# Kernel tuning notes

Measured on AMD Instinct MI355X. Metric: run time of the kernel, lower is better.

## Reference

```python
import jax, jax.numpy as jnp
import numpy as np

N_A = 50000; N_B = 50000          # nodes per type
FD = 8; BINS = 32; EMB = 16       # discrete features, bins, per-feature embed dim
HID = 64; ZD = 32                 # hidden_dim, embed_dim
E = 800000                        # edges per relation (avg degree 16)


def setup_inputs() -> dict:
    key = jax.random.key(0)
    ks = iter(jax.random.split(key, 64))
    def nrm(shape, s=0.05):
        return jax.random.normal(next(ks), shape, jnp.float32) * s
    def ri(shape, hi):
        return jax.random.randint(next(ks), shape, 0, hi, dtype=jnp.int32)
    inp = {
        'x_A': ri((N_A, FD), BINS),
        'x_B': ri((N_B, FD), BINS),
        'ei_ab': ri((2, E), N_A),   # src in A, dst in B (N_A == N_B)
        'ei_ba': ri((2, E), N_B),
        'ei_aa': ri((2, E), N_A),
        # per-feature embedding tables [FD, BINS, EMB]
        'emb_A': nrm((FD, BINS, EMB)), 'emb_B': nrm((FD, BINS, EMB)),
        # pre_lin per node type (in = FD*EMB)
        'pre_W_A': nrm((FD * EMB, HID)), 'pre_b_A': nrm((HID,)),
        'pre_W_B': nrm((FD * EMB, HID)), 'pre_b_B': nrm((HID,)),
        # SAGEConv per relation: lin_l (on aggregated msgs, with bias), lin_r (root, no bias)
        'sage_l_W_ab': nrm((HID, HID)), 'sage_l_b_ab': nrm((HID,)), 'sage_r_W_ab': nrm((HID, HID)),
        'sage_l_W_ba': nrm((HID, HID)), 'sage_l_b_ba': nrm((HID,)), 'sage_r_W_ba': nrm((HID, HID)),
        'sage_l_W_aa': nrm((HID, HID)), 'sage_l_b_aa': nrm((HID,)), 'sage_r_W_aa': nrm((HID, HID)),
        # lin_proj per node type
        'proj_W_A': nrm((HID, ZD)), 'proj_b_A': nrm((ZD,)),
        'proj_W_B': nrm((HID, ZD)), 'proj_b_B': nrm((ZD,)),
        # feature heads per node type -> FD*BINS logits
        'head_W_A': nrm((ZD, FD * BINS)), 'head_b_A': nrm((FD * BINS,)),
        'head_W_B': nrm((ZD, FD * BINS)), 'head_b_B': nrm((FD * BINS,)),
        # bilinear edge decoders per relation: W [1, ZD, ZD], bias [1]
        'bil_W_ab': nrm((1, ZD, ZD)), 'bil_b_ab': nrm((1,)),
        'bil_W_ba': nrm((1, ZD, ZD)), 'bil_b_ba': nrm((1,)),
        'bil_W_aa': nrm((1, ZD, ZD)), 'bil_b_aa': nrm((1,)),
    }
    return inp


def _segment_mean(vals, idx, n):
    s = jax.ops.segment_sum(vals, idx, num_segments=n)
    c = jax.ops.segment_sum(jnp.ones((vals.shape[0], 1), vals.dtype), idx, num_segments=n)
    return s / jnp.maximum(c, 1.0)


def _sage(x_src, x_dst, ei, Wl, bl, Wr):
    # SAGEConv: lin_l(mean_{j in N(i)} x_j) + lin_r(x_i)
    m = _segment_mean(x_src[ei[0]], ei[1], x_dst.shape[0])
    return m @ Wl + bl + x_dst @ Wr


def _embed(x, emb):
    # emb: [FD, BINS, EMB]; x: [N, FD] ints -> [N, FD*EMB]
    e = emb[jnp.arange(FD)[None, :], x]            # [N, FD, EMB]
    return e.reshape(x.shape[0], FD * EMB)


def _bilinear(zs, zd, W, b):
    # nn.Bilinear: out_o = zs^T W_o zd + b_o ; here out dim 1, squeeze
    return (jnp.einsum('ei,oij,ej->eo', zs, W, zd) + b)[:, 0]


def _forward(x_A, x_B, ei_ab, ei_ba, ei_aa,
             emb_A, emb_B, pre_W_A, pre_b_A, pre_W_B, pre_b_B,
             sage_l_W_ab, sage_l_b_ab, sage_r_W_ab,
             sage_l_W_ba, sage_l_b_ba, sage_r_W_ba,
             sage_l_W_aa, sage_l_b_aa, sage_r_W_aa,
             proj_W_A, proj_b_A, proj_W_B, proj_b_B,
             head_W_A, head_b_A, head_W_B, head_b_B,
             bil_W_ab, bil_b_ab, bil_W_ba, bil_b_ba, bil_W_aa, bil_b_aa):
    # feature encoder + pre_lin + relu
    x0_A = jax.nn.relu(_embed(x_A, emb_A) @ pre_W_A + pre_b_A)
    x0_B = jax.nn.relu(_embed(x_B, emb_B) @ pre_W_B + pre_b_B)
    # HeteroConv(SAGEConv per relation, aggr='mean' over relations per dst type)
    h_B = _sage(x0_A, x0_B, ei_ab, sage_l_W_ab, sage_l_b_ab, sage_r_W_ab)
    h_A = (_sage(x0_B, x0_A, ei_ba, sage_l_W_ba, sage_l_b_ba, sage_r_W_ba)
           + _sage(x0_A, x0_A, ei_aa, sage_l_W_aa, sage_l_b_aa, sage_r_W_aa)) * 0.5
    # projection
    z_A = jax.nn.relu(h_A @ proj_W_A + proj_b_A)
    z_B = jax.nn.relu(h_B @ proj_W_B + proj_b_B)
    # feature decode
    fl_A = (z_A @ head_W_A + head_b_A).reshape(-1, FD, BINS)
    fl_B = (z_B @ head_W_B + head_b_B).reshape(-1, FD, BINS)
    # edge decode (bilinear on gathered endpoint embeddings)
    s_ab = _bilinear(z_A[ei_ab[0]], z_B[ei_ab[1]], bil_W_ab, bil_b_ab)
    s_ba = _bilinear(z_B[ei_ba[0]], z_A[ei_ba[1]], bil_W_ba, bil_b_ba)
    s_aa = _bilinear(z_A[ei_aa[0]], z_A[ei_aa[1]], bil_W_aa, bil_b_aa)
    return (z_A, z_B, fl_A, fl_B, s_ab, s_ba, s_aa)


def reference(x_A, x_B, ei_ab, ei_ba, ei_aa,
              emb_A, emb_B, pre_W_A, pre_b_A, pre_W_B, pre_b_B,
              sage_l_W_ab, sage_l_b_ab, sage_r_W_ab,
              sage_l_W_ba, sage_l_b_ba, sage_r_W_ba,
              sage_l_W_aa, sage_l_b_aa, sage_r_W_aa,
              proj_W_A, proj_b_A, proj_W_B, proj_b_B,
              head_W_A, head_b_A, head_W_B, head_b_B,
              bil_W_ab, bil_b_ab, bil_W_ba, bil_b_ba, bil_W_aa, bil_b_aa):
    return _forward(x_A, x_B, ei_ab, ei_ba, ei_aa,
                    emb_A, emb_B, pre_W_A, pre_b_A, pre_W_B, pre_b_B,
                    sage_l_W_ab, sage_l_b_ab, sage_r_W_ab,
                    sage_l_W_ba, sage_l_b_ba, sage_r_W_ba,
                    sage_l_W_aa, sage_l_b_aa, sage_r_W_aa,
                    proj_W_A, proj_b_A, proj_W_B, proj_b_B,
                    head_W_A, head_b_A, head_W_B, head_b_B,
                    bil_W_ab, bil_b_ab, bil_W_ba, bil_b_ba, bil_W_aa, bil_b_aa)
```

## Files before the change

kernel.cpp:

```cpp
#include <hip/hip_runtime.h>

typedef unsigned short u16;
typedef unsigned int u32;
typedef __attribute__((ext_vector_type(8))) short short8;
typedef __attribute__((ext_vector_type(4))) float f32x4;

constexpr int NA = 50000, NB = 50000;
constexpr int EMB = 16, HID = 64;
constexpr int NE = 800000;
constexpr int NBKT = 782;
constexpr int CAPB = 1536;
constexpr int EPB = 8192;
constexpr int BPR = (NE + EPB - 1) / EPB;
constexpr int MSB = 3 * BPR;

#define MFMA16(a, b, c) __builtin_amdgcn_mfma_f32_16x16x32_bf16(a, b, c, 0, 0, 0)

__device__ inline u16 f2bf(float f) {
  u32 b = __float_as_uint(f);
  return (u16)((b + 0x7FFFu + ((b >> 16) & 1u)) >> 16);
}
__device__ inline float bfl(u32 u) { return __uint_as_float(u << 16); }
__device__ inline float bfh(u32 u) { return __uint_as_float(u & 0xFFFF0000u); }
__device__ inline float bfs(u16 u) { return __uint_as_float((u32)u << 16); }

__global__ void __launch_bounds__(256) k_pre(
    const float* __restrict__ embA, const float* __restrict__ embB,
    const float* __restrict__ preWA, const float* __restrict__ preWB,
    float* __restrict__ T,
    const float* __restrict__ Wr_ba, const float* __restrict__ Wr_aa,
    const float* __restrict__ Wl_ba, const float* __restrict__ Wl_aa,
    const float* __restrict__ Wl_ab, const float* __restrict__ Wr_ab,
    const float* __restrict__ bl_ba, const float* __restrict__ bl_aa,
    const float* __restrict__ projWA, const float* __restrict__ projWB,
    const float* __restrict__ headWA, const float* __restrict__ headWB,
    const float* __restrict__ bilW_ba, const float* __restrict__ bilW_aa,
    const float* __restrict__ bilW_ab,
    u16* __restrict__ frag, float* __restrict__ bhA) {
  int blk = blockIdx.x;
  int t = threadIdx.x;

  if (blk < 128) {
    int id = blk * 256 + t;
    int type = id >> 14;
    int rem = id & 16383;
    int fdbin = rem >> 6;
    int col = rem & 63;
    int fd = fdbin >> 5;
    const float* emb = type ? embB : embA;
    const float* W = type ? preWB : preWA;
    const float* e = emb + fdbin * EMB;
    const float* w = W + (fd * EMB) * HID + col;
    float s = 0.f;
#pragma unroll
    for (int j = 0; j < EMB; ++j) s += e[j] * w[j * HID];
    T[id] = s;
    return;
  }

  int tid = (blk - 128) * 256 + t;
  if (tid >= 86 * 64) {
    int i = tid - 86 * 64;
    if (i < 64) bhA[i] = 0.5f * (bl_ba[i] + bl_aa[i]);
    return;
  }
  int f = tid >> 6, lane = tid & 63;
  int nidx = lane & 15, quad = lane >> 4;
  u16* dst = frag + (size_t)f * 512 + lane * 8;
#pragma unroll
  for (int j = 0; j < 8; ++j) {
    int kq = quad * 8 + j;
    float v;
    if (f < 24) {
      int s = f >> 2, nt = f & 3, k = s * 32 + kq, c = nt * 16 + nidx;
      v = (k < 64) ? 0.5f * (Wr_ba[k * 64 + c] + Wr_aa[k * 64 + c])
          : (k < 128) ? 0.5f * Wl_ba[(k - 64) * 64 + c]
                      : 0.5f * Wl_aa[(k - 128) * 64 + c];
    } else if (f < 28) {
      int g = f - 24, k = (g >> 1) * 32 + kq, c = (g & 1) * 16 + nidx;
      v = projWA[k * 32 + c];
    } else if (f < 44) {
      int c = (f - 28) * 16 + nidx;
      v = headWA[kq * 256 + c];
    } else if (f < 46) {
      int i2 = (f - 44) * 16 + nidx;
      v = bilW_ba[i2 * 32 + kq];
    } else if (f < 48) {
      int i2 = (f - 46) * 16 + nidx;
      v = bilW_aa[i2 * 32 + kq];
    } else if (f < 64) {
      int g = f - 48, s = g >> 2, nt = g & 3, k = s * 32 + kq, c = nt * 16 + nidx;
      v = (k < 64) ? Wr_ab[k * 64 + c] : Wl_ab[(k - 64) * 64 + c];
    } else if (f < 68) {
      int g = f - 64, k = (g >> 1) * 32 + kq, c = (g & 1) * 16 + nidx;
      v = projWB[k * 32 + c];
    } else if (f < 84) {
      int c = (f - 68) * 16 + nidx;
      v = headWB[kq * 256 + c];
    } else {
      int i2 = (f - 84) * 16 + nidx;
      v = bilW_ab[i2 * 32 + kq];
    }
    dst[j] = f2bf(v);
  }
}

__global__ void __launch_bounds__(256) k_msx0(
    const int* __restrict__ xA, const int* __restrict__ xB,
    const float* __restrict__ T,
    const float* __restrict__ biasA, const float* __restrict__ biasB,
    u16* __restrict__ x0A, u16* __restrict__ x0B,
    const int* __restrict__ ei_ab, const int* __restrict__ ei_ba,
    const int* __restrict__ ei_aa, int* __restrict__ gcur,
    u32* __restrict__ buckets) {
  __shared__ int hist[NBKT];
  __shared__ int wcur[NBKT];
  int blk = blockIdx.x;
  int t = threadIdx.x;

  if (blk < MSB) {
    int rel = blk / BPR;
    int lb = blk - rel * BPR;
    const int* ei = rel == 0 ? ei_ab : (rel == 1 ? ei_ba : ei_aa);
    int e0 = lb * EPB;
    int n = min(EPB, NE - e0);
    for (int i = t; i < NBKT; i += 256) hist[i] = 0;
    __syncthreads();
    for (int i = t; i < n; i += 256) {
      int dstn = ei[NE + e0 + i];
      atomicAdd(&hist[dstn >> 6], 1);
    }
    __syncthreads();
    for (int i = t; i < NBKT; i += 256) {
      int c = hist[i];
      wcur[i] = (c > 0) ? atomicAdd(&gcur[(rel * NBKT + i) << 4], c) : 0;
    }
    __syncthreads();
    for (int i = t; i < n; i += 256) {
      int src = ei[e0 + i];
      int dstn = ei[NE + e0 + i];
      int b = dstn >> 6;
      int pos = atomicAdd(&wcur[b], 1);
      if (pos < CAPB)
        buckets[(size_t)(rel * NBKT + b) * CAPB + pos] =
            ((u32)src << 6) | (u32)(dstn & 63);
    }
    return;
  }

  int xblk = blk - MSB;
  int type = xblk >= 782;
  int lb = type ? xblk - 782 : xblk;
  const int* x = type ? xB : xA;
  const float4* Tv = (const float4*)(T + (type ? 16384 : 0));
  const float* bias = type ? biasB : biasA;
  u16* x0 = type ? x0B : x0A;
  const int N = NA;

  int r = t >> 2, q = t & 3;
  int row = lb * 64 + r;
  bool valid = row < N;
  int arow = valid ? row : (N - 1);
  const int4* xp = (const int4*)(x + arow * 8);
  int4 xa = xp[0], xb = xp[1];
  int bins[8] = {xa.x, xa.y, xa.z, xa.w, xb.x, xb.y, xb.z, xb.w};
  int c0 = q * 16;
  float acc[16];
#pragma unroll
  for (int j = 0; j < 16; ++j) acc[j] = bias[c0 + j];
#pragma unroll
  for (int fd = 0; fd < 8; ++fd) {
    int base = (fd * 32 + bins[fd]) * 16 + q * 4;
    float4 v0 = Tv[base], v1 = Tv[base + 1], v2 = Tv[base + 2], v3 = Tv[base + 3];
    acc[0] += v0.x;  acc[1] += v0.y;  acc[2] += v0.z;  acc[3] += v0.w;
    acc[4] += v1.x;  acc[5] += v1.y;  acc[6] += v1.z;  acc[7] += v1.w;
    acc[8] += v2.x;  acc[9] += v2.y;  acc[10] += v2.z; acc[11] += v2.w;
    acc[12] += v3.x; acc[13] += v3.y; acc[14] += v3.z; acc[15] += v3.w;
  }
  if (valid) {
    u32 p[8];
#pragma unroll
    for (int j = 0; j < 8; ++j) {
      u16 lo = f2bf(fmaxf(acc[2 * j], 0.f));
      u16 hi = f2bf(fmaxf(acc[2 * j + 1], 0.f));
      p[j] = (u32)lo | ((u32)hi << 16);
    }
    u32* o = (u32*)(x0 + (size_t)row * 64 + c0);
    *(uint4*)o = *(uint4*)&p[0];
    *((uint4*)o + 1) = *(uint4*)&p[4];
  }
}

__global__ void __launch_bounds__(256) k_meansort_all(
    const u32* __restrict__ buckets, const int* __restrict__ cur,
    const u16* __restrict__ x0A, const u16* __restrict__ x0B,
    u16* __restrict__ mab, u16* __restrict__ mba, u16* __restrict__ maa) {
  __shared__ u32 ebuf[CAPB];
  __shared__ u16 csr[CAPB];
  __shared__ int dcnt[64], doff[64], wcur[64];
  int blk = blockIdx.x;
  int rel = blk / NBKT;
  int lb = blk - rel * NBKT;
  int t = threadIdx.x;
  const u16* x0 = (rel == 1) ? x0B : x0A;
  u16* out = rel == 0 ? mab : (rel == 1 ? mba : maa);
  int n = min(cur[blk << 4], CAPB);
  const u32* bk = buckets + (size_t)blk * CAPB;
  if (t < 64) dcnt[t] = 0;
  __syncthreads();
  for (int i = t; i < n; i += 256) {
    u32 v = bk[i];
    ebuf[i] = v;
    atomicAdd(&dcnt[v & 63], 1);
  }
  __syncthreads();
  if (t == 0) {
    int s = 0;
#pragma unroll
    for (int d = 0; d < 64; ++d) {
      doff[d] = s;
      wcur[d] = s;
      s += dcnt[d];
    }
  }
  __syncthreads();
  for (int i = t; i < n; i += 256) {
    u32 v = ebuf[i];
    int p = atomicAdd(&wcur[v & 63], 1);
    csr[p] = (u16)(v >> 6);
  }
  __syncthreads();
  int lane = t & 63, w = t >> 6;
  int g = lane >> 4;
  int dim4 = (lane & 15) * 4;
  int base = lb * 64;
  for (int c = 0; c < 4; ++c) {
    int dloc = w * 16 + c * 4 + g;
    int dstn = base + dloc;
    if (dstn < 50000) {
      int off = doff[dloc], deg = dcnt[dloc];
      float a0 = 0.f, a1 = 0.f, a2 = 0.f, a3 = 0.f;
      int i = 0;
      for (; i + 8 <= deg; i += 8) {
        uint2 v0 = *(const uint2*)(x0 + (size_t)csr[off + i] * 64 + dim4);
        uint2 v1 = *(const uint2*)(x0 + (size_t)csr[off + i + 1] * 64 + dim4);
        uint2 v2 = *(const uint2*)(x0 + (size_t)csr[off + i + 2] * 64 + dim4);
        uint2 v3 = *(const uint2*)(x0 + (size_t)csr[off + i + 3] * 64 + dim4);
        uint2 v4 = *(const uint2*)(x0 + (size_t)csr[off + i + 4] * 64 + dim4);
        uint2 v5 = *(const uint2*)(x0 + (size_t)csr[off + i + 5] * 64 + dim4);
        uint2 v6 = *(const uint2*)(x0 + (size_t)csr[off + i + 6] * 64 + dim4);
        uint2 v7 = *(const uint2*)(x0 + (size_t)csr[off + i + 7] * 64 + dim4);
        a0 += bfl(v0.x) + bfl(v1.x) + bfl(v2.x) + bfl(v3.x) +
              bfl(v4.x) + bfl(v5.x) + bfl(v6.x) + bfl(v7.x);
        a1 += bfh(v0.x) + bfh(v1.x) + bfh(v2.x) + bfh(v3.x) +
              bfh(v4.x) + bfh(v5.x) + bfh(v6.x) + bfh(v7.x);
        a2 += bfl(v0.y) + bfl(v1.y) + bfl(v2.y) + bfl(v3.y) +
              bfl(v4.y) + bfl(v5.y) + bfl(v6.y) + bfl(v7.y);
        a3 += bfh(v0.y) + bfh(v1.y) + bfh(v2.y) + bfh(v3.y) +
              bfh(v4.y) + bfh(v5.y) + bfh(v6.y) + bfh(v7.y);
      }
      for (; i + 4 <= deg; i += 4) {
        uint2 v0 = *(const uint2*)(x0 + (size_t)csr[off + i] * 64 + dim4);
        uint2 v1 = *(const uint2*)(x0 + (size_t)csr[off + i + 1] * 64 + dim4);
        uint2 v2 = *(const uint2*)(x0 + (size_t)csr[off + i + 2] * 64 + dim4);
        uint2 v3 = *(const uint2*)(x0 + (size_t)csr[off + i + 3] * 64 + dim4);
        a0 += bfl(v0.x) + bfl(v1.x) + bfl(v2.x) + bfl(v3.x);
        a1 += bfh(v0.x) + bfh(v1.x) + bfh(v2.x) + bfh(v3.x);
        a2 += bfl(v0.y) + bfl(v1.y) + bfl(v2.y) + bfl(v3.y);
        a3 += bfh(v0.y) + bfh(v1.y) + bfh(v2.y) + bfh(v3.y);
      }
      for (; i < deg; ++i) {
        uint2 v0 = *(const uint2*)(x0 + (size_t)csr[off + i] * 64 + dim4);
        a0 += bfl(v0.x);
        a1 += bfh(v0.x);
        a2 += bfl(v0.y);
        a3 += bfh(v0.y);
      }
      float inv = deg > 0 ? 1.f / (float)deg : 0.f;
      uint2 o;
      o.x = (u32)f2bf(a0 * inv) | ((u32)f2bf(a1 * inv) << 16);
      o.y = (u32)f2bf(a2 * inv) | ((u32)f2bf(a3 * inv) << 16);
      *(uint2*)(out + (size_t)dstn * 64 + dim4) = o;
    }
  }
}

template <int NS, int NY>
__device__ __forceinline__ void node_chain(
    const u16* __restrict__ x0, const u16* __restrict__ m1, const u16* __restrict__ m2,
    const u16* __restrict__ frag, int f1, int f2, int fy, int fh,
    const float* __restrict__ hbias, const float* __restrict__ projb,
    const float* __restrict__ headb,
    float* __restrict__ zout, float* __restrict__ flout,
    u16* __restrict__ zbf, u16* __restrict__ y1bf, u16* __restrict__ y2bf,
    int rows0, int N, u16* hld, u16* zld, int lane) {
  int nidx = lane & 15, quad = lane >> 4;
  size_t r0 = (size_t)min(rows0 + nidx, N - 1);
  size_t r1 = (size_t)min(rows0 + 16 + nidx, N - 1);

  f32x4 acc[2][4];
#pragma unroll
  for (int mt = 0; mt < 2; ++mt)
#pragma unroll
    for (int nt = 0; nt < 4; ++nt) acc[mt][nt] = {0.f, 0.f, 0.f, 0.f};
  const u16* mats[3] = {x0, m1, m2};
#pragma unroll
  for (int s = 0; s < NS; ++s) {
    const u16* src = mats[s >> 1];
    int koff = (s & 1) * 32 + quad * 8;
    short8 a0 = *(const short8*)(src + r0 * 64 + koff);
    short8 a1 = *(const short8*)(src + r1 * 64 + koff);
#pragma unroll
    for (int nt = 0; nt < 4; ++nt) {
      short8 b = *(const short8*)(frag + (size_t)(f1 + s * 4 + nt) * 512 + lane * 8);
      acc[0][nt] = MFMA16(a0, b, acc[0][nt]);
      acc[1][nt] = MFMA16(a1, b, acc[1][nt]);
    }
  }
#pragma unroll
  for (int mt = 0; mt < 2; ++mt)
#pragma unroll
    for (int nt = 0; nt < 4; ++nt) {
      int col = nt * 16 + nidx;
      float bb = hbias[col];
#pragma unroll
      for (int r2 = 0; r2 < 4; ++r2)
        hld[(mt * 16 + quad * 4 + r2) * 72 + col] = f2bf(acc[mt][nt][r2] + bb);
    }

  f32x4 zacc[2][2];
#pragma unroll
  for (int mt = 0; mt < 2; ++mt)
#pragma unroll
    for (int nt = 0; nt < 2; ++nt) zacc[mt][nt] = {0.f, 0.f, 0.f, 0.f};
#pragma unroll
  for (int s = 0; s < 2; ++s) {
    short8 a0 = *(const short8*)(hld + nidx * 72 + s * 32 + quad * 8);
    short8 a1 = *(const short8*)(hld + (16 + nidx) * 72 + s * 32 + quad * 8);
#pragma unroll
    for (int nt = 0; nt < 2; ++nt) {
      short8 b = *(const short8*)(frag + (size_t)(f2 + s * 2 + nt) * 512 + lane * 8);
      zacc[0][nt] = MFMA16(a0, b, zacc[0][nt]);
      zacc[1][nt] = MFMA16(a1, b, zacc[1][nt]);
    }
  }
#pragma unroll
  for (int mt = 0; mt < 2; ++mt)
#pragma unroll
    for (int nt = 0; nt < 2; ++nt) {
      int col = nt * 16 + nidx;
      float pb = projb[col];
#pragma unroll
      for (int r2 = 0; r2 < 4; ++r2) {
        int rl = mt * 16 + quad * 4 + r2;
        float zv = fmaxf(zacc[mt][nt][r2] + pb, 0.f);
        zld[rl * 40 + col] = f2bf(zv);
        int grow = rows0 + rl;
        if (grow < N) zout[(size_t)grow * 32 + col] = zv;
      }
    }
  {
    int rl = lane >> 1, hf = lane & 1;
    int grow = rows0 + rl;
    if (grow < N) {
      short8 v0 = *(const short8*)(zld + rl * 40 + hf * 16);
      short8 v1 = *(const short8*)(zld + rl * 40 + hf * 16 + 8);
      *(short8*)(zbf + (size_t)grow * 32 + hf * 16) = v0;
      *(short8*)(zbf + (size_t)grow * 32 + hf * 16 + 8) = v1;
    }
  }

  short8 az0 = *(const short8*)(zld + nidx * 40 + quad * 8);
  short8 az1 = *(const short8*)(zld + (16 + nidx) * 40 + quad * 8);
#pragma unroll
  for (int mat = 0; mat < NY; ++mat) {
    f32x4 ya[2][2];
#pragma unroll
    for (int mt = 0; mt < 2; ++mt)
#pragma unroll
      for (int nt = 0; nt < 2; ++nt) ya[mt][nt] = {0.f, 0.f, 0.f, 0.f};
#pragma unroll
    for (int nt = 0; nt < 2; ++nt) {
      short8 b = *(const short8*)(frag + (size_t)(fy + mat * 2 + nt) * 512 + lane * 8);
      ya[0][nt] = MFMA16(az0, b, ya[0][nt]);
      ya[1][nt] = MFMA16(az1, b, ya[1][nt]);
    }
#pragma unroll
    for (int mt = 0; mt < 2; ++mt)
#pragma unroll
      for (int nt = 0; nt < 2; ++nt)
#pragma unroll
        for (int r2 = 0; r2 < 4; ++r2)
          hld[(mt * 16 + quad * 4 + r2) * 40 + nt * 16 + nidx] = f2bf(ya[mt][nt][r2]);
    u16* yo = mat ? y2bf : y1bf;
    int rl = lane >> 1, hf = lane & 1;
    int grow = rows0 + rl;
    if (grow < N) {
      short8 v0 = *(const short8*)(hld + rl * 40 + hf * 16);
      short8 v1 = *(const short8*)(hld + rl * 40 + hf * 16 + 8);
      *(short8*)(yo + (size_t)grow * 32 + hf * 16) = v0;
      *(short8*)(yo + (size_t)grow * 32 + hf * 16 + 8) = v1;
    }
  }

  for (int chunk = 0; chunk < 4; ++chunk) {
    f32x4 fa[2][4];
#pragma unroll
    for (int mt = 0; mt < 2; ++mt)
#pragma unroll
      for (int nt = 0; nt < 4; ++nt) fa[mt][nt] = {0.f, 0.f, 0.f, 0.f};
#pragma unroll
    for (int nt = 0; nt < 4; ++nt) {
      short8 b = *(const short8*)(frag + (size_t)(fh + chunk * 4 + nt) * 512 + lane * 8);
      fa[0][nt] = MFMA16(az0, b, fa[0][nt]);
      fa[1][nt] = MFMA16(az1, b, fa[1][nt]);
    }
#pragma unroll
    for (int mt = 0; mt < 2; ++mt)
#pragma unroll
      for (int nt = 0; nt < 4; ++nt) {
        int col = chunk * 64 + nt * 16 + nidx;
        float hb = headb[col];
#pragma unroll
        for (int r2 = 0; r2 < 4; ++r2) {
          int grow = rows0 + mt * 16 + quad * 4 + r2;
          if (grow < N) flout[(size_t)grow * 256 + col] = fa[mt][nt][r2] + hb;
        }
      }
  }
}

__global__ void __launch_bounds__(256) k_node(
    const u16* __restrict__ x0A, const u16* __restrict__ mba, const u16* __restrict__ maa,
    const u16* __restrict__ x0B, const u16* __restrict__ mab,
    const u16* __restrict__ frag, const float* __restrict__ bhA,
    const float* __restrict__ bl_ab,
    const float* __restrict__ projbA, const float* __restrict__ headbA,
    const float* __restrict__ projbB, const float* __restrict__ headbB,
    float* __restrict__ zA, float* __restrict__ flA, u16* __restrict__ zAbf,
    u16* __restrict__ ybabf, u16* __restrict__ yaabf,
    float* __restrict__ zB, float* __restrict__ flB, u16* __restrict__ zBbf,
    u16* __restrict__ yabbf) {
  __shared__ u16 lds[4][3584];
  int t = threadIdx.x, lane = t & 63, w = t >> 6;
  u16* hld = &lds[w][0];
  u16* zld = &lds[w][2304];
  int blk = blockIdx.x;
  if (blk < 391) {
    node_chain<6, 2>(x0A, mba, maa, frag, 0, 24, 44, 28, bhA, projbA, headbA,
                     zA, flA, zAbf, ybabf, yaabf, blk * 128 + w * 32, NA, hld, zld, lane);
  } else {
    node_chain<4, 1>(x0B, mab, mab, frag, 48, 64, 84, 68, bl_ab, projbB, headbB,
                     zB, flB, zBbf, yabbf, yabbf, (blk - 391) * 128 + w * 32, NB, hld,
                     zld, lane);
  }
}

__global__ void k_bil_all(const int* __restrict__ ei_ab, const int* __restrict__ ei_ba,
                          const int* __restrict__ ei_aa,
                          const u16* __restrict__ zA, const u16* __restrict__ zB,
                          const u16* __restrict__ yab, const u16* __restrict__ yba,
                          const u16* __restrict__ yaa,
                          const float* __restrict__ b_ab, const float* __restrict__ b_ba,
                          const float* __restrict__ b_aa,
                          float* __restrict__ s_ab, float* __restrict__ s_ba,
                          float* __restrict__ s_aa) {
  int e = blockIdx.x * 256 + threadIdx.x;
  int rel = e / NE;
  int le = e - rel * NE;
  const int* ei = rel == 0 ? ei_ab : (rel == 1 ? ei_ba : ei_aa);
  const u16* zs = (rel == 1) ? zB : zA;
  const u16* yd = rel == 0 ? yab : (rel == 1 ? yba : yaa);
  const float* bb = rel == 0 ? b_ab : (rel == 1 ? b_ba : b_aa);
  float* so = rel == 0 ? s_ab : (rel == 1 ? s_ba : s_aa);
  int si = ei[le], di = ei[NE + le];
  const uint4* zp = (const uint4*)(zs + (size_t)si * 32);
  const uint4* yp = (const uint4*)(yd + (size_t)di * 32);
  float acc = 0.f;
#pragma unroll
  for (int i = 0; i < 4; ++i) {
    uint4 a = zp[i], c = yp[i];
    acc += bfl(a.x) * bfl(c.x) + bfh(a.x) * bfh(c.x);
    acc += bfl(a.y) * bfl(c.y) + bfh(a.y) * bfh(c.y);
    acc += bfl(a.z) * bfl(c.z) + bfh(a.z) * bfh(c.z);
    acc += bfl(a.w) * bfl(c.w) + bfh(a.w) * bfh(c.w);
  }
  so[le] = acc + bb[0];
}

extern "C" void kernel_launch(void* const* d_in, const int* in_sizes, int n_in,
                              void* d_out, int out_size, void* d_ws, size_t ws_size,
                              hipStream_t stream) {
  const int* xA = (const int*)d_in[0];
  const int* xB = (const int*)d_in[1];
  const int* ei_ab = (const int*)d_in[2];
  const int* ei_ba = (const int*)d_in[3];
  const int* ei_aa = (const int*)d_in[4];
  const float* embA = (const float*)d_in[5];
  const float* embB = (const float*)d_in[6];
  const float* preWA = (const float*)d_in[7];
  const float* prebA = (const float*)d_in[8];
  const float* preWB = (const float*)d_in[9];
  const float* prebB = (const float*)d_in[10];
  const float* Wl_ab = (const float*)d_in[11];
  const float* bl_ab = (const float*)d_in[12];
  const float* Wr_ab = (const float*)d_in[13];
  const float* Wl_ba = (const float*)d_in[14];
  const float* bl_ba = (const float*)d_in[15];
  const float* Wr_ba = (const float*)d_in[16];
  const float* Wl_aa = (const float*)d_in[17];
  const float* bl_aa = (const float*)d_in[18];
  const float* Wr_aa = (const float*)d_in[19];
  const float* projWA = (const float*)d_in[20];
  const float* projbA = (const float*)d_in[21];
  const float* projWB = (const float*)d_in[22];
  const float* projbB = (const float*)d_in[23];
  const float* headWA = (const float*)d_in[24];
  const float* headbA = (const float*)d_in[25];
  const float* headWB = (const float*)d_in[26];
  const float* headbB = (const float*)d_in[27];
  const float* bilW_ab = (const float*)d_in[28];
  const float* bilb_ab = (const float*)d_in[29];
  const float* bilW_ba = (const float*)d_in[30];
  const float* bilb_ba = (const float*)d_in[31];
  const float* bilW_aa = (const float*)d_in[32];
  const float* bilb_aa = (const float*)d_in[33];

  float* out = (float*)d_out;
  float* zA = out;
  float* zB = out + 1600000;
  float* flA = out + 3200000;
  float* flB = out + 16000000;
  float* s_ab = out + 28800000;
  float* s_ba = out + 29600000;
  float* s_aa = out + 30400000;

  char* ws = (char*)d_ws;
  float* T = (float*)(ws + 0);
  u16* x0Abf = (u16*)(ws + 131072);
  u16* x0Bbf = (u16*)(ws + 6531072);
  u16* mabbf = (u16*)(ws + 12931072);
  u16* mbabf = (u16*)(ws + 19331072);
  u16* maabf = (u16*)(ws + 25731072);
  u16* zAbf = (u16*)(ws + 32131072);
  u16* zBbf = (u16*)(ws + 35331072);
  u16* yabbf = (u16*)(ws + 38531072);
  u16* ybabf = (u16*)(ws + 41731072);
  u16* yaabf = (u16*)(ws + 44931072);
  int* cur = (int*)(ws + 48131072);
  u16* frag = (u16*)(ws + 48731072);
  float* bhA = (float*)(ws + 48819136);

  u32* buckets = (u32*)flA;

  hipMemsetAsync(cur, 0, 3 * NBKT * 64, stream);
  k_pre<<<150, 256, 0, stream>>>(
      embA, embB, preWA, preWB, T,
      Wr_ba, Wr_aa, Wl_ba, Wl_aa, Wl_ab, Wr_ab, bl_ba, bl_aa,
      projWA, projWB, headWA, headWB, bilW_ba, bilW_aa, bilW_ab,
      frag, bhA);
  k_msx0<<<MSB + 2 * 782, 256, 0, stream>>>(
      xA, xB, T, prebA, prebB, x0Abf, x0Bbf,
      ei_ab, ei_ba, ei_aa, cur, buckets);
  k_meansort_all<<<3 * NBKT, 256, 0, stream>>>(buckets, cur, x0Abf, x0Bbf,
                                               mabbf, mbabf, maabf);
  k_node<<<782, 256, 0, stream>>>(x0Abf, mbabf, maabf, x0Bbf, mabbf, frag, bhA,
                                  bl_ab, projbA, headbA, projbB, headbB,
                                  zA, flA, zAbf, ybabf, yaabf, zB, flB, zBbf, yabbf);
  k_bil_all<<<3 * NE / 256, 256, 0, stream>>>(ei_ab, ei_ba, ei_aa, zAbf, zBbf,
                                              yabbf, ybabf, yaabf,
                                              bilb_ab, bilb_ba, bilb_aa,
                                              s_ab, s_ba, s_aa);
}
```

Before: 392.8 us.

## Locally sort edges by bucket in shared memory before coalesced bucket writes

The edge bucketing phase now computes a block-wide prefix scan of the bucket histogram, scatters packed edges into a shared-memory buffer ordered by bucket, and then writes them out in contiguous runs so consecutive threads store to adjacent global addresses instead of scattering randomly. The per-bucket global counters are also packed densely rather than padded to 64-byte stride, which shrinks the memset. It adds a 32KB shared buffer plus a scan with several barriers, which may lower occupancy of the bucketing blocks, and contended global atomics on the now-adjacent counters may rise.

```diff
diff --git a/kernel.cpp b/kernel.cpp
--- a/kernel.cpp
+++ b/kernel.cpp
@@ -113,8 +113,11 @@
     const int* __restrict__ ei_ab, const int* __restrict__ ei_ba,
     const int* __restrict__ ei_aa, int* __restrict__ gcur,
     u32* __restrict__ buckets) {
+  __shared__ u32 ebuf2[EPB];
   __shared__ int hist[NBKT];
-  __shared__ int wcur[NBKT];
+  __shared__ int loff[NBKT];
+  __shared__ int delta[NBKT];
+  __shared__ int scanw[256];
   int blk = blockIdx.x;
   int t = threadIdx.x;
 
@@ -131,19 +134,54 @@
       atomicAdd(&hist[dstn >> 6], 1);
     }
     __syncthreads();
+    int base4 = t * 4;
+    int s = 0;
+#pragma unroll
+    for (int k = 0; k < 4; ++k) {
+      int idx = base4 + k;
+      if (idx < NBKT) s += hist[idx];
+    }
+    scanw[t] = s;
+    __syncthreads();
+    for (int off = 1; off < 256; off <<= 1) {
+      int v = (t >= off) ? scanw[t - off] : 0;
+      __syncthreads();
+      scanw[t] += v;
+      __syncthreads();
+    }
+    int run = (t == 0) ? 0 : scanw[t - 1];
+#pragma unroll
+    for (int k = 0; k < 4; ++k) {
+      int idx = base4 + k;
+      if (idx < NBKT) {
+        loff[idx] = run;
+        run += hist[idx];
+      }
+    }
+    __syncthreads();
     for (int i = t; i < NBKT; i += 256) {
       int c = hist[i];
-      wcur[i] = (c > 0) ? atomicAdd(&gcur[(rel * NBKT + i) << 4], c) : 0;
+      if (c > 0) {
+        int g = atomicAdd(&gcur[rel * NBKT + i], c);
+        delta[i] = g - loff[i];
+      }
+      hist[i] = loff[i];
     }
     __syncthreads();
     for (int i = t; i < n; i += 256) {
       int src = ei[e0 + i];
       int dstn = ei[NE + e0 + i];
       int b = dstn >> 6;
-      int pos = atomicAdd(&wcur[b], 1);
-      if (pos < CAPB)
-        buckets[(size_t)(rel * NBKT + b) * CAPB + pos] =
-            ((u32)src << 6) | (u32)(dstn & 63);
+      int p = atomicAdd(&hist[b], 1);
+      ebuf2[p] = ((u32)b << 22) | ((u32)src << 6) | (u32)(dstn & 63);
+    }
+    __syncthreads();
+    for (int j = t; j < n; j += 256) {
+      u32 v = ebuf2[j];
+      int b = v >> 22;
+      int gpos = delta[b] + j;
+      if (gpos < CAPB)
+        buckets[(size_t)(rel * NBKT + b) * CAPB + gpos] = v & 0x3FFFFFu;
     }
     return;
   }
@@ -204,7 +242,7 @@
   int t = threadIdx.x;
   const u16* x0 = (rel == 1) ? x0B : x0A;
   u16* out = rel == 0 ? mab : (rel == 1 ? mba : maa);
-  int n = min(cur[blk << 4], CAPB);
+  int n = min(cur[blk], CAPB);
   const u32* bk = buckets + (size_t)blk * CAPB;
   if (t < 64) dcnt[t] = 0;
   __syncthreads();
@@ -553,7 +591,7 @@
 
   u32* buckets = (u32*)flA;
 
-  hipMemsetAsync(cur, 0, 3 * NBKT * 64, stream);
+  hipMemsetAsync(cur, 0, 3 * NBKT * sizeof(int), stream);
   k_pre<<<150, 256, 0, stream>>>(
       embA, embB, preWA, preWB, T,
       Wr_ba, Wr_aa, Wl_ba, Wl_aa, Wl_ab, Wr_ab, bl_ba, bl_aa,
```

After: 362.7 us. 1.08x faster.
